# Optimization experiments

Hardware: AMD Instinct MI355X
Metric: run time of the kernel (lower is better)

## Reference

```python
import jax, jax.numpy as jnp
import numpy as np

M, L, Q = 512, 256, 21


def setup_inputs() -> dict:
    key = jax.random.key(0)
    k1, k2, k3 = jax.random.split(key, 3)
    # one-hot encoded sequences (M, L, q)
    X_idx = jax.random.randint(k1, (M, L), 0, Q)
    X_oh = jax.nn.one_hot(X_idx, Q, dtype=jnp.float32)
    h_pos = 0.01 * jax.random.normal(k2, (L, Q), dtype=jnp.float32)
    J = 0.01 * jax.random.normal(k3, (L, L, Q, Q), dtype=jnp.float32)
    return {"X_oh": X_oh, "h_pos": h_pos, "J": J}


def reference(X_oh, h_pos, J):
    # z[m,i,a] = h[i,a] + sum_{j<i} sum_b J[i,j,b,a] * X[m,j,b]
    # (matches torch einsum 'mpq,pqr->mpr' over tril-gathered blocks)
    L_, q_ = h_pos.shape
    i_idx, j_idx = jnp.tril_indices(L_, k=-1)          # (P,), strictly lower, i sorted
    J_blocks = J[i_idx, j_idx]                          # (P, q, q)
    X_blocks = X_oh[:, j_idx]                           # (M, P, q)
    contrib = jnp.einsum('mpb,pba->mpa', X_blocks, J_blocks)  # (M, P, q)
    # scatter-add contributions to their target position i (sorted segments)
    agg = jax.ops.segment_sum(
        jnp.swapaxes(contrib, 0, 1),                    # (P, M, q)
        i_idx, num_segments=L_, indices_are_sorted=True
    )                                                   # (L, M, q)
    return h_pos[None, :, :] + jnp.swapaxes(agg, 0, 1)  # (M, L, q)
```

## Files before the change

### kernel.cpp

```cpp
#include <hip/hip_runtime.h>

#define Q_DIM 21
#define BLKB  1764
#define WINB  1792
#define SLOT  2304
#define NBUF  16
#define DEPTH 12

#define GLD(src, dst, sz) __builtin_amdgcn_global_load_lds( \
    (const __attribute__((address_space(1))) void*)(src),   \
    (__attribute__((address_space(3))) void*)(dst), sz, 0, 0)

__global__ __launch_bounds__(64) void ardca_prep(const float* __restrict__ X_oh,
                                                 unsigned short* __restrict__ Xt) {
  int w = blockIdx.x;
  int lane = threadIdx.x;
  const float* base = X_oh + (size_t)w * (32 * Q_DIM);
  int rowbase = w * 32;
#pragma unroll
  for (int p = 0; p < 11; ++p) {
    int f = p * 63 + lane;
    float v = (lane < 63 && f < 672) ? base[f] : 0.0f;
    unsigned long long mask = __ballot(v > 0.5f);
    if (lane < 3) {
      int rloc = 3 * p + lane;
      if (rloc < 32) {
        unsigned int bits = (unsigned int)((mask >> (21 * lane)) & 0x1FFFFFu);
        int x = bits ? __builtin_ctz(bits) : 0;
        int rr = rowbase + rloc;
        int m = rr >> 8, j = rr & 255;
        Xt[j * 512 + m] = (unsigned short)(x * 84);
      }
    }
  }
}

template <int USE_XT>
__global__ __launch_bounds__(512, 4) void ardca_main(const float* __restrict__ Jm,
                                                     const float* __restrict__ h,
                                                     const unsigned short* __restrict__ Xt,
                                                     const float* __restrict__ X_oh,
                                                     float* __restrict__ out) {
  alignas(16) __shared__ char lds[NBUF * SLOT];
  int b = blockIdx.x;
  int i, mh;
  if (b < 256) { i = b; mh = 0; }
  else { int x = b - 256; i = 248 - (x & ~7) + (x & 7); mh = 1; }
  int tid = threadIdx.x;
  int ml = tid & 255;
  int ah = tid >> 8;
  int m = mh * 256 + ml;

  const char* Jrow = (const char*)Jm + (size_t)i * (256ull * BLKB);
  const char* XtB  = (const char*)Xt;

  const float* hp = h + i * Q_DIM + ah * 12;
  float acc[12];
#pragma unroll
  for (int k = 0; k < 12; ++k)
    acc[k] = (k < 9 || ah == 0) ? hp[k] : 0.0f;

  auto STAGE = [&](int j) {
    char* buf = lds + (j & (NBUF - 1)) * SLOT;
    unsigned bb = (unsigned)j * BLKB;
    const char* src = Jrow + (bb & ~15u);
    if (tid < 112) GLD(src + tid * 16, buf + tid * 16, 16);
    if (USE_XT) {
      if (tid >= 128 && tid < 160)
        GLD(XtB + j * 1024 + mh * 512 + (tid - 128) * 16,
            buf + WINB + (tid - 128) * 16, 16);
    }
  };

  auto CONSUME = [&](int j) {
    const char* buf = lds + (j & (NBUF - 1)) * SLOT;
    int off;
    if (USE_XT) {
      off = *(const unsigned short*)(buf + WINB + 2 * ml);
    } else {
      const float* p = X_oh + ((size_t)m * 256 + j) * Q_DIM;
      int x = 0;
#pragma unroll
      for (int a = 0; a < Q_DIM; ++a) x = (p[a] > 0.5f) ? a : x;
      off = x * 84;
    }
    const float* row = (const float*)(buf + ((j & 3) << 2) + off + ah * 48);
#pragma unroll
    for (int k = 0; k < 12; ++k)
      if (ah == 0 || k < 9) acc[k] += row[k];
  };

  int P = (i < DEPTH) ? i : DEPTH;
  for (int j = 0; j < P; ++j) STAGE(j);
  int jt = i - DEPTH; if (jt < 0) jt = 0;

#pragma unroll 1
  for (int j = 0; j < jt; ++j) {
    STAGE(j + DEPTH);
    if (USE_XT) asm volatile("s_waitcnt vmcnt(12)" ::: "memory");
    else        asm volatile("s_waitcnt vmcnt(0)" ::: "memory");
    __builtin_amdgcn_sched_barrier(0);
    __builtin_amdgcn_s_barrier();
    CONSUME(j);
  }
  asm volatile("s_waitcnt vmcnt(0)" ::: "memory");
  __builtin_amdgcn_sched_barrier(0);
  __builtin_amdgcn_s_barrier();
#pragma unroll 1
  for (int j = jt; j < i; ++j) CONSUME(j);

  float* o = out + ((size_t)m * 256 + i) * Q_DIM + ah * 12;
  if (ah == 0) {
#pragma unroll
    for (int k = 0; k < 12; ++k) o[k] = acc[k];
  } else {
#pragma unroll
    for (int k = 0; k < 9; ++k) o[k] = acc[k];
  }
}

extern "C" void kernel_launch(void* const* d_in, const int* in_sizes, int n_in,
                              void* d_out, int out_size, void* d_ws, size_t ws_size,
                              hipStream_t stream) {
  const float* X_oh = (const float*)d_in[0];
  const float* h    = (const float*)d_in[1];
  const float* Jm   = (const float*)d_in[2];
  float* out        = (float*)d_out;
  unsigned short* Xt = (unsigned short*)d_ws;

  if (ws_size >= 262144) {
    ardca_prep<<<4096, 64, 0, stream>>>(X_oh, Xt);
    ardca_main<1><<<512, 512, 0, stream>>>(Jm, h, Xt, X_oh, out);
  } else {
    ardca_main<0><<<512, 512, 0, stream>>>(Jm, h, Xt, X_oh, out);
  }
}
```

Before: 217.0 us.

## Give each thread all 21 outputs and batch four pipeline steps per barrier

The main kernel drops from 512 to 256 threads per block. Each thread now accumulates all 21 output channels for its sequence, where before two threads split the channels 12/9. The staged loop now issues four J/Xt block loads and waits on one barrier per four positions, and reads four offsets before the gathers to expose more independent LDS loads. This cuts barrier count and duplicated offset reads, but leaves fewer waves to hide latency and raises per-thread register use.

```diff
diff --git a/kernel.cpp b/kernel.cpp
--- a/kernel.cpp
+++ b/kernel.cpp
@@ -5,7 +5,7 @@
 #define WINB  1792
 #define SLOT  2304
 #define NBUF  16
-#define DEPTH 12
+#define AHEAD 12
 
 #define GLD(src, dst, sz) __builtin_amdgcn_global_load_lds( \
     (const __attribute__((address_space(1))) void*)(src),   \
@@ -36,7 +36,7 @@
 }
 
 template <int USE_XT>
-__global__ __launch_bounds__(512, 4) void ardca_main(const float* __restrict__ Jm,
+__global__ __launch_bounds__(256, 2) void ardca_main(const float* __restrict__ Jm,
                                                      const float* __restrict__ h,
                                                      const unsigned short* __restrict__ Xt,
                                                      const float* __restrict__ X_oh,
@@ -47,18 +47,14 @@
   if (b < 256) { i = b; mh = 0; }
   else { int x = b - 256; i = 248 - (x & ~7) + (x & 7); mh = 1; }
   int tid = threadIdx.x;
-  int ml = tid & 255;
-  int ah = tid >> 8;
-  int m = mh * 256 + ml;
+  int m = mh * 256 + tid;
 
   const char* Jrow = (const char*)Jm + (size_t)i * (256ull * BLKB);
   const char* XtB  = (const char*)Xt;
 
-  const float* hp = h + i * Q_DIM + ah * 12;
-  float acc[12];
+  float acc[Q_DIM];
 #pragma unroll
-  for (int k = 0; k < 12; ++k)
-    acc[k] = (k < 9 || ah == 0) ? hp[k] : 0.0f;
+  for (int k = 0; k < Q_DIM; ++k) acc[k] = 0.0f;
 
   auto STAGE = [&](int j) {
     char* buf = lds + (j & (NBUF - 1)) * SLOT;
@@ -72,51 +68,48 @@
     }
   };
 
-  auto CONSUME = [&](int j) {
+  auto OFF = [&](int j) -> int {
     const char* buf = lds + (j & (NBUF - 1)) * SLOT;
-    int off;
-    if (USE_XT) {
-      off = *(const unsigned short*)(buf + WINB + 2 * ml);
-    } else {
-      const float* p = X_oh + ((size_t)m * 256 + j) * Q_DIM;
-      int x = 0;
+    if (USE_XT) return *(const unsigned short*)(buf + WINB + 2 * tid);
+    const float* p = X_oh + ((size_t)m * 256 + j) * Q_DIM;
+    int x = 0;
 #pragma unroll
-      for (int a = 0; a < Q_DIM; ++a) x = (p[a] > 0.5f) ? a : x;
-      off = x * 84;
-    }
-    const float* row = (const float*)(buf + ((j & 3) << 2) + off + ah * 48);
-#pragma unroll
-    for (int k = 0; k < 12; ++k)
-      if (ah == 0 || k < 9) acc[k] += row[k];
+    for (int a = 0; a < Q_DIM; ++a) x = (p[a] > 0.5f) ? a : x;
+    return x * 84;
   };
 
-  int P = (i < DEPTH) ? i : DEPTH;
-  for (int j = 0; j < P; ++j) STAGE(j);
-  int jt = i - DEPTH; if (jt < 0) jt = 0;
+  auto GATHER = [&](int j, int off) {
+    const char* buf = lds + (j & (NBUF - 1)) * SLOT;
+    const float* row = (const float*)(buf + ((j & 3) << 2) + off);
+#pragma unroll
+    for (int k = 0; k < Q_DIM; ++k) acc[k] += row[k];
+  };
 
+  int pre = (i < AHEAD) ? i : AHEAD;
+  for (int j = 0; j < pre; ++j) STAGE(j);
+
+  int jb = 0;
 #pragma unroll 1
-  for (int j = 0; j < jt; ++j) {
-    STAGE(j + DEPTH);
+  for (; jb + 15 < i; jb += 4) {
+    STAGE(jb + 12); STAGE(jb + 13); STAGE(jb + 14); STAGE(jb + 15);
     if (USE_XT) asm volatile("s_waitcnt vmcnt(12)" ::: "memory");
     else        asm volatile("s_waitcnt vmcnt(0)" ::: "memory");
     __builtin_amdgcn_sched_barrier(0);
     __builtin_amdgcn_s_barrier();
-    CONSUME(j);
+    int o0 = OFF(jb), o1 = OFF(jb + 1), o2 = OFF(jb + 2), o3 = OFF(jb + 3);
+    GATHER(jb, o0); GATHER(jb + 1, o1); GATHER(jb + 2, o2); GATHER(jb + 3, o3);
   }
+  for (int j = jb + AHEAD; j < i; ++j) STAGE(j);
   asm volatile("s_waitcnt vmcnt(0)" ::: "memory");
   __builtin_amdgcn_sched_barrier(0);
   __builtin_amdgcn_s_barrier();
 #pragma unroll 1
-  for (int j = jt; j < i; ++j) CONSUME(j);
+  for (int j = jb; j < i; ++j) { int o = OFF(j); GATHER(j, o); }
 
-  float* o = out + ((size_t)m * 256 + i) * Q_DIM + ah * 12;
-  if (ah == 0) {
+  const float* hp = h + i * Q_DIM;
+  float* o = out + ((size_t)m * 256 + i) * Q_DIM;
 #pragma unroll
-    for (int k = 0; k < 12; ++k) o[k] = acc[k];
-  } else {
-#pragma unroll
-    for (int k = 0; k < 9; ++k) o[k] = acc[k];
-  }
+  for (int k = 0; k < Q_DIM; ++k) o[k] = acc[k] + hp[k];
 }
 
 extern "C" void kernel_launch(void* const* d_in, const int* in_sizes, int n_in,
@@ -130,8 +123,8 @@
 
   if (ws_size >= 262144) {
     ardca_prep<<<4096, 64, 0, stream>>>(X_oh, Xt);
-    ardca_main<1><<<512, 512, 0, stream>>>(Jm, h, Xt, X_oh, out);
+    ardca_main<1><<<512, 256, 0, stream>>>(Jm, h, Xt, X_oh, out);
   } else {
-    ardca_main<0><<<512, 512, 0, stream>>>(Jm, h, Xt, X_oh, out);
+    ardca_main<0><<<512, 256, 0, stream>>>(Jm, h, Xt, X_oh, out);
   }
 }
```

Measured after the change: 209.6 us. -3.4%, faster.
